# Kernel optimization log

Measured on AMD Instinct MI355X. Metric: run time of the kernel, lower is better.

The kernel has to match this reference:

```python
import jax, jax.numpy as jnp
import numpy as np

ALPHA, GAMMA, THRESHOLD, NUM_CLASSES = 0.5, 1.5, 0.5, 21
EPS8, EPS7 = 1e-8, 1e-7


def corner_to_center(b):
    w = b[..., 2] - b[..., 0]
    h = b[..., 3] - b[..., 1]
    cx = b[..., 0] + w / 2
    cy = b[..., 1] + h / 2
    return jnp.stack([cx, cy, w, h], axis=-1)


def box_iou(b1, b2):
    # b1: [P,4], b2: [M,4] -> [P,M]
    area1 = (b1[:, 2] - b1[:, 0]) * (b1[:, 3] - b1[:, 1])
    area2 = (b2[:, 2] - b2[:, 0]) * (b2[:, 3] - b2[:, 1])
    lt = jnp.maximum(b1[:, None, :2], b2[None, :, :2])
    rb = jnp.minimum(b1[:, None, 2:], b2[None, :, 2:])
    wh = jnp.clip(rb - lt, 0)
    inter = wh[..., 0] * wh[..., 1]
    return inter / (area1[:, None] + area2[None, :] - inter)


def encode_boxes(matched, dbox):
    g = corner_to_center(matched)
    d = corner_to_center(dbox)
    ex = (g[..., 0] - d[..., 0]) / (d[..., 2] + EPS8)
    ey = (g[..., 1] - d[..., 1]) / (d[..., 3] + EPS8)
    ew = jnp.log(g[..., 2] / (d[..., 2] + EPS8) + EPS8)
    eh = jnp.log(g[..., 3] / (d[..., 3] + EPS8) + EPS8)
    return jnp.stack([ex, ey, ew, eh], axis=-1)


def decode_boxes(loc, dbox):
    d = corner_to_center(dbox)
    cx = loc[..., 0] * d[..., 2] + d[..., 0]
    cy = loc[..., 1] * d[..., 3] + d[..., 1]
    w = jnp.exp(loc[..., 2]) * d[..., 2]
    h = jnp.exp(loc[..., 3]) * d[..., 3]
    return jnp.stack([cx - w / 2, cy - h / 2, cx + w / 2, cy + h / 2], axis=-1)


def giou_loss(pred, tgt):
    inter_min = jnp.maximum(pred[..., :2], tgt[..., :2])
    inter_max = jnp.minimum(pred[..., 2:], tgt[..., 2:])
    inter_wh = jnp.clip(inter_max - inter_min, 0)
    inter = inter_wh[..., 0] * inter_wh[..., 1]
    pa = (pred[..., 2] - pred[..., 0]) * (pred[..., 3] - pred[..., 1])
    ta = (tgt[..., 2] - tgt[..., 0]) * (tgt[..., 3] - tgt[..., 1])
    union = pa + ta - inter
    iou = inter / (union + EPS7)
    encl_min = jnp.minimum(pred[..., :2], tgt[..., :2])
    encl_max = jnp.maximum(pred[..., 2:], tgt[..., 2:])
    encl_wh = jnp.clip(encl_max - encl_min, 0)
    encl = encl_wh[..., 0] * encl_wh[..., 1]
    giou = iou - (encl - union) / (encl + EPS7)
    return 1.0 - giou


def _match_one(truths, labels, dbox):
    # truths: [M,4], labels: [M], dbox: [P,4]
    M = truths.shape[0]
    overlaps = box_iou(dbox, truths)               # [P,M]
    bt_ov = overlaps.max(axis=1)                   # [P]
    bt_idx = overlaps.argmax(axis=1)               # [P]
    bp_idx = overlaps.argmax(axis=0)               # [M] best prior per GT
    # force-match each GT to its best prior
    bt_idx = bt_idx.at[bp_idx].set(jnp.arange(M))
    bt_ov = bt_ov.at[bp_idx].set(2.0)
    matches = truths[bt_idx]                       # [P,4]
    mlabels = jnp.where(bt_ov < THRESHOLD, 0, labels[bt_idx])
    loc_t = encode_boxes(matches, dbox)
    return loc_t, mlabels


def focal_loss(pred, target):
    # pred: [N,C], target: [N]
    logp = jax.nn.log_softmax(pred, axis=-1)
    ce = -jnp.take_along_axis(logp, target[:, None], axis=1)[:, 0]
    p_t = jnp.exp(-ce)
    return ALPHA * (1.0 - p_t) ** GAMMA * ce


def setup_inputs() -> dict:
    key = jax.random.key(0)
    k1, k2, k3, k4, k5, k6, k7 = jax.random.split(key, 7)
    B, P, M, C = 64, 24564, 50, 21
    # valid corner-format boxes: min + positive wh
    d_min = jax.random.uniform(k1, (P, 2)) * 0.8
    d_wh = 0.05 + jax.random.uniform(k2, (P, 2)) * 0.2
    default_boxes = jnp.concatenate([d_min, d_min + d_wh], axis=1)
    g_min = jax.random.uniform(k3, (B, M, 2)) * 0.8
    g_wh = 0.05 + jax.random.uniform(k4, (B, M, 2)) * 0.2
    gt_boxes = jnp.concatenate([g_min, g_min + g_wh], axis=2)
    loc_preds = jax.random.normal(k5, (B, P, 4)) * 0.1
    conf_preds = jax.random.normal(k6, (B, P, C))
    gt_labels = jax.random.randint(k7, (B, M), 1, C)
    return {"loc_preds": loc_preds, "conf_preds": conf_preds,
            "default_boxes": default_boxes, "gt_boxes": gt_boxes,
            "gt_labels": gt_labels}


def reference(loc_preds, conf_preds, default_boxes, gt_boxes, gt_labels):
    B, P, _ = loc_preds.shape
    loc_t, conf_t = jax.vmap(_match_one, in_axes=(0, 0, None))(gt_boxes, gt_labels, default_boxes)
    pos = conf_t > 0                                   # [B,P]
    num_pos = pos.sum()
    denom = jnp.maximum(num_pos, 1).astype(loc_preds.dtype)
    # localization: decode preds and targets against anchors, GIoU on positives
    decoded_pred = decode_boxes(loc_preds, default_boxes[None])
    decoded_tgt = decode_boxes(loc_t, default_boxes[None])
    gl = giou_loss(decoded_pred, decoded_tgt)          # [B,P]
    loc_loss = jnp.sum(jnp.where(pos, gl, 0.0)) / denom
    # classification: focal loss over all anchors
    fl = focal_loss(conf_preds.reshape(-1, conf_preds.shape[-1]), conf_t.reshape(-1))
    conf_loss = fl.sum() / denom
    total = loc_loss + conf_loss
    return jnp.where(num_pos == 0, 0.0, total)
```

## Files before the change

### kernel.cpp

```cpp
#include <hip/hip_runtime.h>
#include <cstdint>
#include <cstddef>

#define F_ALPHA 0.5f
#define THRESH  0.5f
#define EPS8    1e-8f
#define EPS7    1e-7f
#define MAXM    64
#define CCLS    21

__global__ void init_kernel(unsigned long long* __restrict__ bpkey, int n)
{
    int i = blockIdx.x * 256 + threadIdx.x;
    if (i < n) bpkey[i] = 0x00000000FFFFFFFFull;
}

__global__ __launch_bounds__(256)
void match_kernel(const float4* __restrict__ dbox,
                  const float4* __restrict__ gt,
                  unsigned long long* __restrict__ bpkey,
                  unsigned char* __restrict__ match,
                  int P, int M)
{
    __shared__ float4 tb[MAXM];
    __shared__ float  tarea[MAXM];
    __shared__ unsigned long long wkey[MAXM][4];

    const int t    = threadIdx.x;
    const int b    = blockIdx.y;
    const int p    = blockIdx.x * 256 + t;
    const bool valid = (p < P);
    const int w    = t >> 6;
    const int lane = t & 63;

    if (t < M) {
        float4 g = gt[(size_t)b * M + t];
        tb[t] = g;
        tarea[t] = (g.z - g.x) * (g.w - g.y);
    }
    __syncthreads();

    float4 d = valid ? dbox[p] : make_float4(9.f, 9.f, 9.f, 9.f);
    const float darea = (d.z - d.x) * (d.w - d.y);

    float best = -1.0f;
    int   bm = 0;

    const unsigned pbase = blockIdx.x * 256 + (unsigned)(w << 6);

    #pragma unroll 2
    for (int m = 0; m < M; ++m) {
        float4 g = tb[m];
        float ta = tarea[m];
        float lx = fmaxf(d.x, g.x), ly = fmaxf(d.y, g.y);
        float rx = fminf(d.z, g.z), ry = fminf(d.w, g.w);
        float iw = fmaxf(rx - lx, 0.f), ih = fmaxf(ry - ly, 0.f);
        float inter = iw * ih;
        float iou = inter * __builtin_amdgcn_rcpf(darea + ta - inter);

        if (iou > best) { best = iou; bm = m; }

        float v = iou;
        v = fmaxf(v, __shfl_xor(v,  1, 64));
        v = fmaxf(v, __shfl_xor(v,  2, 64));
        v = fmaxf(v, __shfl_xor(v,  4, 64));
        v = fmaxf(v, __shfl_xor(v,  8, 64));
        v = fmaxf(v, __shfl_xor(v, 16, 64));
        v = fmaxf(v, __shfl_xor(v, 32, 64));

        unsigned long long k;
        if (v > 0.0f) {
            unsigned long long mb = __ballot(iou == v);
            unsigned wl = (unsigned)(__ffsll((unsigned long long)mb) - 1);
            unsigned pp = pbase + wl;
            k = ((unsigned long long)__float_as_uint(v) << 32)
                | (unsigned long long)(0xFFFFFFFFu - pp);
        } else {
            k = 0x00000000FFFFFFFFull;
        }
        if (lane == 0) wkey[m][w] = k;
    }
    __syncthreads();

    if (t < M) {
        unsigned long long k0 = wkey[t][0], k1 = wkey[t][1];
        unsigned long long k2 = wkey[t][2], k3 = wkey[t][3];
        unsigned long long ka = (k0 > k1) ? k0 : k1;
        unsigned long long kb = (k2 > k3) ? k2 : k3;
        unsigned long long k  = (ka > kb) ? ka : kb;
        if (k >> 32) atomicMax(&bpkey[(size_t)b * M + t], k);
    }

    if (valid) {
        unsigned char code = (unsigned char)((best >= THRESH ? 0x40 : 0) | bm);
        match[(size_t)b * P + p] = code;
    }
}

__global__ __launch_bounds__(256)
void loss_kernel(const float4* __restrict__ locp,
                 const float*  __restrict__ conf,
                 const float4* __restrict__ dbox,
                 const float4* __restrict__ gt,
                 const int*    __restrict__ gtl,
                 const unsigned long long* __restrict__ bpkey,
                 const unsigned char* __restrict__ match,
                 double* __restrict__ partS,
                 int*    __restrict__ partC,
                 int P, int M)
{
    __shared__ float    scf[256 * CCLS];
    __shared__ float4   tb[MAXM];
    __shared__ int      tl[MAXM];
    __shared__ unsigned bpp[MAXM];
    __shared__ double   sv[4];
    __shared__ int      sc[4];

    const int t = threadIdx.x;
    const int b = blockIdx.y;
    const int p0 = blockIdx.x * 256;
    const int p = p0 + t;

    if (t < M) {
        tb[t] = gt[(size_t)b * M + t];
        tl[t] = gtl[(size_t)b * M + t];
        bpp[t] = 0xFFFFFFFFu - (unsigned)(bpkey[(size_t)b * M + t] & 0xFFFFFFFFull);
    }

    const int cnt = min(256, P - p0);
    const int nf = cnt * CCLS;
    const float* src = conf + ((size_t)b * P + p0) * CCLS;
    if (((uintptr_t)src & 15) == 0) {
        const int n4 = nf >> 2;
        const float4* s4 = (const float4*)src;
        float4* d4 = (float4*)scf;
        for (int i = t; i < n4; i += 256) d4[i] = s4[i];
        for (int i = (n4 << 2) + t; i < nf; i += 256) scf[i] = src[i];
    } else {
        for (int i = t; i < nf; i += 256) scf[i] = src[i];
    }
    __syncthreads();

    double acc = 0.0;
    int cnt_pos = 0;
    if (p < P) {
        unsigned char code = match[(size_t)b * P + p];
        int  idx = code & 0x3F;
        bool pos = (code & 0x40) != 0;
        for (int j = 0; j < M; j++) {
            if (bpp[j] == (unsigned)p) { idx = j; pos = true; }
        }
        int lbl = pos ? tl[idx] : 0;

        const float* x = scf + t * CCLS;
        float mx = -1e30f;
        #pragma unroll
        for (int c = 0; c < CCLS; c++) mx = fmaxf(mx, x[c]);
        float sum = 0.f;
        #pragma unroll
        for (int c = 0; c < CCLS; c++) sum += expf(x[c] - mx);
        float ce = (mx + logf(sum)) - x[lbl];
        float pt = expf(-ce);
        float om = 1.f - pt;
        acc = (double)(F_ALPHA * om * sqrtf(om) * ce);

        if (pos) {
            cnt_pos = 1;
            float4 d = dbox[p];
            float dw = d.z - d.x, dh = d.w - d.y;
            float dcx = d.x + dw * 0.5f, dcy = d.y + dh * 0.5f;
            float4 g = tb[idx];
            float gw = g.z - g.x, gh = g.w - g.y;
            float gcx = g.x + gw * 0.5f, gcy = g.y + gh * 0.5f;
            float ex = (gcx - dcx) / (dw + EPS8);
            float ey = (gcy - dcy) / (dh + EPS8);
            float ew = logf(gw / (dw + EPS8) + EPS8);
            float eh = logf(gh / (dh + EPS8) + EPS8);
            float tcx = ex * dw + dcx, tcy = ey * dh + dcy;
            float tw = expf(ew) * dw,  th = expf(eh) * dh;
            float t0 = tcx - tw * 0.5f, t1 = tcy - th * 0.5f;
            float t2 = tcx + tw * 0.5f, t3 = tcy + th * 0.5f;
            float4 l = locp[(size_t)b * P + p];
            float pcx = l.x * dw + dcx, pcy = l.y * dh + dcy;
            float pw = expf(l.z) * dw,  ph = expf(l.w) * dh;
            float q0 = pcx - pw * 0.5f, q1 = pcy - ph * 0.5f;
            float q2 = pcx + pw * 0.5f, q3 = pcy + ph * 0.5f;
            float ix0 = fmaxf(q0, t0), iy0 = fmaxf(q1, t1);
            float ix1 = fminf(q2, t2), iy1 = fminf(q3, t3);
            float iw = fmaxf(ix1 - ix0, 0.f), ih = fmaxf(iy1 - iy0, 0.f);
            float inter = iw * ih;
            float pa = (q2 - q0) * (q3 - q1);
            float ta = (t2 - t0) * (t3 - t1);
            float uni = pa + ta - inter;
            float iou = inter / (uni + EPS7);
            float e0 = fminf(q0, t0), e1 = fminf(q1, t1);
            float e2 = fmaxf(q2, t2), e3 = fmaxf(q3, t3);
            float ewd = fmaxf(e2 - e0, 0.f), ehd = fmaxf(e3 - e1, 0.f);
            float encl = ewd * ehd;
            float giou = iou - (encl - uni) / (encl + EPS7);
            acc += (double)(1.f - giou);
        }
    }

    for (int o = 32; o > 0; o >>= 1) {
        acc += __shfl_down(acc, o, 64);
        cnt_pos += __shfl_down(cnt_pos, o, 64);
    }
    int w = t >> 6, lane = t & 63;
    if (lane == 0) { sv[w] = acc; sc[w] = cnt_pos; }
    __syncthreads();
    if (t == 0) {
        int slot = blockIdx.y * gridDim.x + blockIdx.x;
        partS[slot] = sv[0] + sv[1] + sv[2] + sv[3];
        partC[slot] = sc[0] + sc[1] + sc[2] + sc[3];
    }
}

__global__ __launch_bounds__(256)
void final_kernel(const double* __restrict__ partS,
                  const int*    __restrict__ partC,
                  float* __restrict__ out, int n)
{
    __shared__ double sv[4];
    __shared__ long long sc[4];
    const int t = threadIdx.x;
    double a = 0.0; long long c = 0;
    for (int i = t; i < n; i += 256) { a += partS[i]; c += partC[i]; }
    for (int o = 32; o > 0; o >>= 1) {
        a += __shfl_down(a, o, 64);
        c += __shfl_down(c, o, 64);
    }
    int w = t >> 6, lane = t & 63;
    if (lane == 0) { sv[w] = a; sc[w] = c; }
    __syncthreads();
    if (t == 0) {
        double s = sv[0] + sv[1] + sv[2] + sv[3];
        long long np = sc[0] + sc[1] + sc[2] + sc[3];
        out[0] = (np == 0) ? 0.0f : (float)(s / (double)np);
    }
}

extern "C" void kernel_launch(void* const* d_in, const int* in_sizes, int n_in,
                              void* d_out, int out_size, void* d_ws, size_t ws_size,
                              hipStream_t stream)
{
    const float* locp = (const float*)d_in[0];
    const float* conf = (const float*)d_in[1];
    const float* dbox = (const float*)d_in[2];
    const float* gt   = (const float*)d_in[3];
    const int*   gtl  = (const int*)d_in[4];

    const int P  = in_sizes[2] / 4;
    const long long BP = (long long)in_sizes[0] / 4;
    const int B  = (int)(BP / P);
    const int M  = in_sizes[4] / B;

    const int nblk = (P + 255) / 256;
    const int nPart = nblk * B;

    char* ws = (char*)d_ws;
    unsigned long long* bpkey = (unsigned long long*)ws;
    size_t off = ((size_t)B * M * 8 + 15) & ~(size_t)15;
    double* partS = (double*)(ws + off);
    off += (size_t)nPart * 8;
    int* partC = (int*)(ws + off);
    off += (size_t)nPart * 4;
    off = (off + 15) & ~(size_t)15;
    unsigned char* match = (unsigned char*)(ws + off);

    dim3 grid(nblk, B);
    init_kernel<<<(B * M + 255) / 256, 256, 0, stream>>>(bpkey, B * M);
    match_kernel<<<grid, 256, 0, stream>>>((const float4*)dbox, (const float4*)gt,
                                           bpkey, match, P, M);
    loss_kernel<<<grid, 256, 0, stream>>>((const float4*)locp, conf,
                                          (const float4*)gt  == nullptr ? (const float4*)dbox : (const float4*)dbox,
                                          (const float4*)gt,
                                          gtl, bpkey, match, partS, partC, P, M);
    final_kernel<<<1, 256, 0, stream>>>(partS, partC, (float*)d_out, nPart);
}
```

Before: 336.2 us.

## Split matching into per-GT best-prior kernel and fuse per-prior match into loss

Replaces the init and per-prior match kernels with a bp_kernel in which each block owns four GT boxes, scans all priors and reduces a packed 64-bit key without atomics. The per-prior best-GT IoU argmax is recomputed inside the loss kernel, so the match byte array no longer goes through global memory. This removes one launch, the atomics and the match round trip. In exchange, bp_kernel's grid is only M/4 × B blocks, each serially scanning all P priors, which may underuse the GPU when P is large.

New measurement: 301.2 us. -10.4%, faster.

```diff
diff --git a/kernel.cpp b/kernel.cpp
--- a/kernel.cpp
+++ b/kernel.cpp
@@ -8,92 +8,72 @@
 #define EPS7    1e-7f
 #define MAXM    64
 #define CCLS    21
-
-__global__ void init_kernel(unsigned long long* __restrict__ bpkey, int n)
-{
-    int i = blockIdx.x * 256 + threadIdx.x;
-    if (i < n) bpkey[i] = 0x00000000FFFFFFFFull;
-}
+#define GGRP    4
 
 __global__ __launch_bounds__(256)
-void match_kernel(const float4* __restrict__ dbox,
-                  const float4* __restrict__ gt,
-                  unsigned long long* __restrict__ bpkey,
-                  unsigned char* __restrict__ match,
-                  int P, int M)
-{
-    __shared__ float4 tb[MAXM];
-    __shared__ float  tarea[MAXM];
-    __shared__ unsigned long long wkey[MAXM][4];
-
-    const int t    = threadIdx.x;
-    const int b    = blockIdx.y;
-    const int p    = blockIdx.x * 256 + t;
-    const bool valid = (p < P);
-    const int w    = t >> 6;
-    const int lane = t & 63;
-
-    if (t < M) {
-        float4 g = gt[(size_t)b * M + t];
-        tb[t] = g;
-        tarea[t] = (g.z - g.x) * (g.w - g.y);
-    }
-    __syncthreads();
-
-    float4 d = valid ? dbox[p] : make_float4(9.f, 9.f, 9.f, 9.f);
-    const float darea = (d.z - d.x) * (d.w - d.y);
-
-    float best = -1.0f;
-    int   bm = 0;
-
-    const unsigned pbase = blockIdx.x * 256 + (unsigned)(w << 6);
-
-    #pragma unroll 2
-    for (int m = 0; m < M; ++m) {
-        float4 g = tb[m];
-        float ta = tarea[m];
-        float lx = fmaxf(d.x, g.x), ly = fmaxf(d.y, g.y);
-        float rx = fminf(d.z, g.z), ry = fminf(d.w, g.w);
-        float iw = fmaxf(rx - lx, 0.f), ih = fmaxf(ry - ly, 0.f);
-        float inter = iw * ih;
-        float iou = inter * __builtin_amdgcn_rcpf(darea + ta - inter);
-
-        if (iou > best) { best = iou; bm = m; }
-
-        float v = iou;
-        v = fmaxf(v, __shfl_xor(v,  1, 64));
-        v = fmaxf(v, __shfl_xor(v,  2, 64));
-        v = fmaxf(v, __shfl_xor(v,  4, 64));
-        v = fmaxf(v, __shfl_xor(v,  8, 64));
-        v = fmaxf(v, __shfl_xor(v, 16, 64));
-        v = fmaxf(v, __shfl_xor(v, 32, 64));
-
-        unsigned long long k;
-        if (v > 0.0f) {
-            unsigned long long mb = __ballot(iou == v);
-            unsigned wl = (unsigned)(__ffsll((unsigned long long)mb) - 1);
-            unsigned pp = pbase + wl;
-            k = ((unsigned long long)__float_as_uint(v) << 32)
-                | (unsigned long long)(0xFFFFFFFFu - pp);
-        } else {
-            k = 0x00000000FFFFFFFFull;
-        }
-        if (lane == 0) wkey[m][w] = k;
-    }
-    __syncthreads();
-
-    if (t < M) {
+void bp_kernel(const float4* __restrict__ dbox,
+               const float4* __restrict__ gt,
+               unsigned* __restrict__ bp,
+               int P, int M)
+{
+    __shared__ unsigned long long wkey[GGRP][4];
+
+    const int b  = blockIdx.y;
+    const int m0 = blockIdx.x * GGRP;
+    const int t  = threadIdx.x;
+    const int w  = t >> 6, lane = t & 63;
+
+    float4 gb[GGRP]; float ga[GGRP];
+    #pragma unroll
+    for (int g = 0; g < GGRP; g++) {
+        int m = min(m0 + g, M - 1);
+        float4 gg = gt[(size_t)b * M + m];
+        gb[g] = gg;
+        ga[g] = (gg.z - gg.x) * (gg.w - gg.y);
+    }
+
+    float    bestv[GGRP];
+    unsigned bestp[GGRP];
+    #pragma unroll
+    for (int g = 0; g < GGRP; g++) { bestv[g] = 0.f; bestp[g] = 0u; }
+
+    for (int p = t; p < P; p += 256) {
+        float4 d = dbox[p];
+        float darea = (d.z - d.x) * (d.w - d.y);
+        #pragma unroll
+        for (int g = 0; g < GGRP; g++) {
+            float4 gg = gb[g];
+            float lx = fmaxf(d.x, gg.x), ly = fmaxf(d.y, gg.y);
+            float rx = fminf(d.z, gg.z), ry = fminf(d.w, gg.w);
+            float iw = fmaxf(rx - lx, 0.f), ih = fmaxf(ry - ly, 0.f);
+            float inter = iw * ih;
+            float iou = inter * __builtin_amdgcn_rcpf(darea + ga[g] - inter);
+            if (iou > bestv[g]) { bestv[g] = iou; bestp[g] = (unsigned)p; }
+        }
+    }
+
+    #pragma unroll
+    for (int g = 0; g < GGRP; g++) {
+        unsigned long long k =
+            ((unsigned long long)__float_as_uint(bestv[g]) << 32)
+            | (unsigned long long)(0xFFFFFFFFu - bestp[g]);
+        #pragma unroll
+        for (int o = 1; o < 64; o <<= 1) {
+            unsigned long long k2 = __shfl_xor(k, o, 64);
+            if (k2 > k) k = k2;
+        }
+        if (lane == 0) wkey[g][w] = k;
+    }
+    __syncthreads();
+    if (t < GGRP) {
         unsigned long long k0 = wkey[t][0], k1 = wkey[t][1];
         unsigned long long k2 = wkey[t][2], k3 = wkey[t][3];
         unsigned long long ka = (k0 > k1) ? k0 : k1;
         unsigned long long kb = (k2 > k3) ? k2 : k3;
         unsigned long long k  = (ka > kb) ? ka : kb;
-        if (k >> 32) atomicMax(&bpkey[(size_t)b * M + t], k);
-    }
-
-    if (valid) {
-        unsigned char code = (unsigned char)((best >= THRESH ? 0x40 : 0) | bm);
-        match[(size_t)b * P + p] = code;
+        int m = m0 + t;
+        if (m < M)
+            bp[(size_t)b * M + m] = 0xFFFFFFFFu - (unsigned)(k & 0xFFFFFFFFull);
     }
 }
 
@@ -103,14 +83,14 @@
                  const float4* __restrict__ dbox,
                  const float4* __restrict__ gt,
                  const int*    __restrict__ gtl,
-                 const unsigned long long* __restrict__ bpkey,
-                 const unsigned char* __restrict__ match,
+                 const unsigned* __restrict__ bp,
                  double* __restrict__ partS,
                  int*    __restrict__ partC,
                  int P, int M)
 {
     __shared__ float    scf[256 * CCLS];
     __shared__ float4   tb[MAXM];
+    __shared__ float    tarea[MAXM];
     __shared__ int      tl[MAXM];
     __shared__ unsigned bpp[MAXM];
     __shared__ double   sv[4];
@@ -122,9 +102,11 @@
     const int p = p0 + t;
 
     if (t < M) {
-        tb[t] = gt[(size_t)b * M + t];
+        float4 g = gt[(size_t)b * M + t];
+        tb[t] = g;
+        tarea[t] = (g.z - g.x) * (g.w - g.y);
         tl[t] = gtl[(size_t)b * M + t];
-        bpp[t] = 0xFFFFFFFFu - (unsigned)(bpkey[(size_t)b * M + t] & 0xFFFFFFFFull);
+        bpp[t] = bp[(size_t)b * M + t];
     }
 
     const int cnt = min(256, P - p0);
@@ -144,9 +126,24 @@
     double acc = 0.0;
     int cnt_pos = 0;
     if (p < P) {
-        unsigned char code = match[(size_t)b * P + p];
-        int  idx = code & 0x3F;
-        bool pos = (code & 0x40) != 0;
+        float4 d = dbox[p];
+        const float dw_ = d.z - d.x, dh_ = d.w - d.y;
+        const float darea = dw_ * dh_;
+
+        float best = -1.0f;
+        int   bm = 0;
+        for (int m = 0; m < M; m++) {
+            float4 g = tb[m];
+            float lx = fmaxf(d.x, g.x), ly = fmaxf(d.y, g.y);
+            float rx = fminf(d.z, g.z), ry = fminf(d.w, g.w);
+            float iw = fmaxf(rx - lx, 0.f), ih = fmaxf(ry - ly, 0.f);
+            float inter = iw * ih;
+            float iou = inter * __builtin_amdgcn_rcpf(darea + tarea[m] - inter);
+            if (iou > best) { best = iou; bm = m; }
+        }
+
+        int  idx = bm;
+        bool pos = (best >= THRESH);
         for (int j = 0; j < M; j++) {
             if (bpp[j] == (unsigned)p) { idx = j; pos = true; }
         }
@@ -166,8 +163,7 @@
 
         if (pos) {
             cnt_pos = 1;
-            float4 d = dbox[p];
-            float dw = d.z - d.x, dh = d.w - d.y;
+            float dw = dw_, dh = dh_;
             float dcx = d.x + dw * 0.5f, dcy = d.y + dh * 0.5f;
             float4 g = tb[idx];
             float gw = g.z - g.x, gh = g.w - g.y;
@@ -259,22 +255,18 @@
     const int nPart = nblk * B;
 
     char* ws = (char*)d_ws;
-    unsigned long long* bpkey = (unsigned long long*)ws;
-    size_t off = ((size_t)B * M * 8 + 15) & ~(size_t)15;
+    unsigned* bp = (unsigned*)ws;
+    size_t off = ((size_t)B * M * 4 + 15) & ~(size_t)15;
     double* partS = (double*)(ws + off);
     off += (size_t)nPart * 8;
     int* partC = (int*)(ws + off);
-    off += (size_t)nPart * 4;
-    off = (off + 15) & ~(size_t)15;
-    unsigned char* match = (unsigned char*)(ws + off);
-
+
+    dim3 gridBP((M + GGRP - 1) / GGRP, B);
     dim3 grid(nblk, B);
-    init_kernel<<<(B * M + 255) / 256, 256, 0, stream>>>(bpkey, B * M);
-    match_kernel<<<grid, 256, 0, stream>>>((const float4*)dbox, (const float4*)gt,
-                                           bpkey, match, P, M);
+    bp_kernel<<<gridBP, 256, 0, stream>>>((const float4*)dbox, (const float4*)gt,
+                                          bp, P, M);
     loss_kernel<<<grid, 256, 0, stream>>>((const float4*)locp, conf,
-                                          (const float4*)gt  == nullptr ? (const float4*)dbox : (const float4*)dbox,
-                                          (const float4*)gt,
-                                          gtl, bpkey, match, partS, partC, P, M);
+                                          (const float4*)dbox, (const float4*)gt,
+                                          gtl, bp, partS, partC, P, M);
     final_kernel<<<1, 256, 0, stream>>>(partS, partC, (float*)d_out, nPart);
 }
```
